# Optimization experiments

Measured on AMD Instinct MI355X. Metric: run time of the kernel, lower is better.

Reference implementation:

```python
import jax, jax.numpy as jnp
import numpy as np

K_NN = 4  # hard-coded k in get_graph_feature(x, k=4)


def _conv1(h, Wm, s, b):
    # 1x1 conv1d + folded-BN (scale/shift) + ReLU
    return jax.nn.relu(jnp.einsum('oc,bcn->bon', Wm, h) * s[:, None] + b[:, None])


def _conv2(h, Wm, s, b):
    # 1x1 conv2d + folded-BN + ReLU
    return jax.nn.relu(jnp.einsum('oc,bcnk->bonk', Wm, h) * s[:, None, None] + b[:, None, None])


def _forward(x, W_dup, s_dup, b_dup, W_c1, s_c1, b_c1,
             W2a, s2a, b2a, W2b, s2b, b2b, W2c, s2c, b2c,
             W3a, s3a, b3a, W3b, s3b, b3b, W4a, bias4a, W4b, bias4b):
    B = x.shape[0]
    h = _conv1(x, W_dup, s_dup, b_dup)           # (B,256,1024)
    h = h.reshape(B, 128, 2048)                  # duplicate points: (B,128,2048)
    h = _conv1(h, W_c1, s_c1, b_c1)              # (B,64,2048)
    g = jnp.max(h, axis=2, keepdims=True)        # max_pool1d over all 2048 -> (B,64,1)
    # knn on 64-d features: pairwise = -||xi-xj||^2, topk picks nearest (self included)
    xx = jnp.sum(h * h, axis=1, keepdims=True)   # (B,1,P)
    inner = -2.0 * jnp.einsum('bcn,bcm->bnm', h, h)
    pd = -xx - inner - jnp.swapaxes(xx, 1, 2)    # (B,P,P)
    idx = jax.lax.top_k(pd, K_NN)[1]             # (B,P,k)
    xt = jnp.swapaxes(h, 1, 2)                   # (B,P,C)
    nb = xt[jnp.arange(B)[:, None, None], idx]   # gather neighbors: (B,P,k,C)
    ctr = xt[:, :, None, :]
    feat = jnp.concatenate([nb - ctr, jnp.broadcast_to(ctr, nb.shape)], axis=-1)  # (B,P,k,2C)
    feat = jnp.transpose(feat, (0, 3, 1, 2))     # (B,128,P,k)
    feat = _conv2(feat, W2a, s2a, b2a)
    feat = _conv2(feat, W2b, s2b, b2b)
    feat = _conv2(feat, W2c, s2c, b2c)           # (B,64,P,k)
    local = jnp.max(feat, axis=3)                # max over k -> (B,64,P)
    g = _conv1(g, W3a, s3a, b3a)
    g = _conv1(g, W3b, s3b, b3b)                 # (B,128,1)
    final = jnp.concatenate([local, jnp.broadcast_to(g, (B, 128, local.shape[2]))], axis=1)  # (B,192,P)
    h4 = jax.nn.relu(jnp.einsum('oc,bcn->bon', W4a, final) + bias4a[:, None])  # (B,256,P)
    out = jnp.einsum('oc,bcn->bon', W4b, h4) + bias4b[:, None]                 # (B,3,P)
    return out


def setup_inputs() -> dict:
    key = jax.random.key(0)
    ks = list(jax.random.split(key, 30))
    W = lambda k, o, c: jax.random.normal(k, (o, c), jnp.float32) * 0.05
    sc = lambda k, c: 1.0 + 0.1 * jax.random.normal(k, (c,), jnp.float32)
    bs = lambda k, c: 0.1 * jax.random.normal(k, (c,), jnp.float32)
    return {
        'search_keypoint': jax.random.normal(ks[0], (8, 128, 1024), jnp.float32),
        'W_dup': W(ks[1], 256, 128), 's_dup': sc(ks[2], 256), 'b_dup': bs(ks[3], 256),
        'W_c1': W(ks[4], 64, 128), 's_c1': sc(ks[5], 64), 'b_c1': bs(ks[6], 64),
        'W2a': W(ks[7], 64, 128), 's2a': sc(ks[8], 64), 'b2a': bs(ks[9], 64),
        'W2b': W(ks[10], 64, 64), 's2b': sc(ks[11], 64), 'b2b': bs(ks[12], 64),
        'W2c': W(ks[13], 64, 64), 's2c': sc(ks[14], 64), 'b2c': bs(ks[15], 64),
        'W3a': W(ks[16], 128, 64), 's3a': sc(ks[17], 128), 'b3a': bs(ks[18], 128),
        'W3b': W(ks[19], 128, 128), 's3b': sc(ks[20], 128), 'b3b': bs(ks[21], 128),
        'W4a': W(ks[22], 256, 192), 'bias4a': bs(ks[23], 256),
        'W4b': W(ks[24], 3, 256), 'bias4b': bs(ks[25], 3),
    }


def reference(search_keypoint, W_dup, s_dup, b_dup, W_c1, s_c1, b_c1,
              W2a, s2a, b2a, W2b, s2b, b2b, W2c, s2c, b2c,
              W3a, s3a, b3a, W3b, s3b, b3b, W4a, bias4a, W4b, bias4b):
    return _forward(search_keypoint, W_dup, s_dup, b_dup, W_c1, s_c1, b_c1,
                    W2a, s2a, b2a, W2b, s2b, b2b, W2c, s2c, b2c,
                    W3a, s3a, b3a, W3b, s3b, b3b, W4a, bias4a, W4b, bias4b)
```

## Files before the change

kernel.cpp:

```cpp
#include <hip/hip_runtime.h>
#include <float.h>

typedef __attribute__((ext_vector_type(8))) short short8;
typedef __attribute__((ext_vector_type(4))) float f32x4;
typedef unsigned short u16;
typedef unsigned long long u64;

static constexpr size_t OFF_W     = 0;
static constexpr size_t OFF_YZ    = 131072;
static constexpr size_t OFF_Zf    = 1179648;
static constexpr size_t OFF_FEATR = 2228224;
static constexpr size_t OFF_FIN   = 6422528;
static constexpr size_t OFF_XX    = 9568256;
static constexpr size_t OFF_G     = 9584640;
static constexpr size_t OFF_G4    = 9617408;
static constexpr size_t WS_FLOATS = 9652736;

static constexpr size_t WO_DUP = 0;
static constexpr size_t WO_C1  = 32768;
static constexpr size_t WO_2A  = 40960;
static constexpr size_t WO_2B  = 49152;
static constexpr size_t WO_2C  = 53248;
static constexpr size_t WO_4A  = 57344;

__device__ __forceinline__ void gl_lds16(const void* g, void* l) {
    __builtin_amdgcn_global_load_lds(
        (const __attribute__((address_space(1))) void*)g,
        (__attribute__((address_space(3))) void*)l, 16, 0, 0);
}

__device__ __forceinline__ u16 f2bf(float x) {
    union { float f; unsigned int u; } v; v.f = x;
    unsigned int r = v.u + 0x7fffu + ((v.u >> 16) & 1u);
    return (u16)(r >> 16);
}
__device__ __forceinline__ float bf2f(u16 h) {
    union { unsigned int u; float f; } v; v.u = ((unsigned int)h) << 16;
    return v.f;
}
__device__ __forceinline__ void split2(float x, u16& h, u16& l) {
    h = f2bf(x);
    l = f2bf(x - bf2f(h));
}

__device__ __forceinline__ unsigned int fmap(float f) {
    unsigned int u = __float_as_uint(f);
    return u ^ ((unsigned int)((int)u >> 31) | 0x80000000u);
}
__device__ __forceinline__ u64 mkkey(float f, int m) {
    return ((u64)fmap(f) << 32) | (unsigned int)(2047 - m);
}
static __device__ __forceinline__ void ins4k(u64 k, u64 bk[4])
{
#pragma unroll
    for (int s = 0; s < 4; ++s) {
        bool better = k > bk[s];
        u64 t = bk[s];
        bk[s] = better ? k : bk[s];
        k = better ? t : k;
    }
}

__global__ __launch_bounds__(256) void prep(
    const float* __restrict__ W_dup, const float* __restrict__ W_c1,
    const float* __restrict__ W2a, const float* __restrict__ W2b,
    const float* __restrict__ W2c, const float* __restrict__ W4a,
    const float* __restrict__ x,
    u16* __restrict__ whi, u16* __restrict__ wlo,
    u16* __restrict__ xthi, u16* __restrict__ xtlo)
{
    __shared__ float tile[64][65];
    if (blockIdx.x < 416) {
        int t = blockIdx.x * 256 + threadIdx.x;
        float v;
        if      (t < 40960) v = (t < 32768) ? W_dup[t] : W_c1[t - 32768];
        else if (t < 53248) v = (t < 49152) ? W2a[t - 40960] : W2b[t - 49152];
        else                v = (t < 57344) ? W2c[t - 53248] : W4a[t - 57344];
        u16 h, l; split2(v, h, l);
        whi[t] = h; wlo[t] = l;
    } else {
        const int bb = blockIdx.x - 416;
        const int n0 = (bb & 15) * 64;
        const int c0 = ((bb >> 4) & 1) * 64;
        const int b  = bb >> 5;
        const int t  = threadIdx.x;
        const float* xb = x + ((size_t)b * 128 + c0) * 1024;
#pragma unroll
        for (int i = 0; i < 16; ++i) {
            int c = i * 4 + (t >> 6), n = t & 63;
            tile[c][n] = xb[(size_t)c * 1024 + n0 + n];
        }
        __syncthreads();
#pragma unroll
        for (int i = 0; i < 16; ++i) {
            int n = i * 4 + (t >> 6), c = t & 63;
            u16 h, l; split2(tile[c][n], h, l);
            const size_t o = ((size_t)b * 1024 + n0 + n) * 128 + c0 + c;
            xthi[o] = h; xtlo[o] = l;
        }
    }
}

__global__ __launch_bounds__(512) void backbone(
    const u16* __restrict__ xthi, const u16* __restrict__ xtlo,
    const u16* __restrict__ whi, const u16* __restrict__ wlo,
    const float* __restrict__ s_dup, const float* __restrict__ b_dup,
    const float* __restrict__ s_c1, const float* __restrict__ b_c1,
    u16* __restrict__ h2thi, u16* __restrict__ h2tlo,
    float* __restrict__ xxb, float* __restrict__ gp,
    float* __restrict__ y, float* __restrict__ z)
{
    const int t = threadIdx.x;
    const int wu = t >> 6;
    const int lane = t & 63;
    const int j = lane & 15, q = lane >> 4;
    const int nb = blockIdx.x;
    const int b  = blockIdx.y;
    const int n0 = nb * 16;

    __shared__ __align__(16) u16 h1h[32 * 136], h1l[32 * 136];
    __shared__ __align__(16) u16 h2h[32 * 72],  h2l[32 * 72];
    __shared__ float xxp[2][4][16];
    __shared__ float gpart[2][64];

    {
        const size_t arow = ((size_t)b * 1024 + n0 + j) * 128;
        short8 ahv[4], alv[4];
#pragma unroll
        for (int ks = 0; ks < 4; ++ks) {
            ahv[ks] = *(const short8*)(xthi + arow + q * 8 + ks * 32);
            alv[ks] = *(const short8*)(xtlo + arow + q * 8 + ks * 32);
        }
        const u16* wdh = whi + WO_DUP;
        const u16* wdl = wlo + WO_DUP;
#pragma unroll
        for (int ci = 0; ci < 2; ++ci) {
            const int ctile = wu * 2 + ci;
            const int o = ctile * 16 + j;
            f32x4 acc = (f32x4){0.f, 0.f, 0.f, 0.f};
#pragma unroll
            for (int ks = 0; ks < 4; ++ks) {
                short8 bh = *(const short8*)(wdh + (size_t)o * 128 + q * 8 + ks * 32);
                short8 bl = *(const short8*)(wdl + (size_t)o * 128 + q * 8 + ks * 32);
                acc = __builtin_amdgcn_mfma_f32_16x16x32_bf16(ahv[ks], bh, acc, 0, 0, 0);
                acc = __builtin_amdgcn_mfma_f32_16x16x32_bf16(ahv[ks], bl, acc, 0, 0, 0);
                acc = __builtin_amdgcn_mfma_f32_16x16x32_bf16(alv[ks], bh, acc, 0, 0, 0);
            }
            const float sc = s_dup[o], bi = b_dup[o];
            const int lrbase = (j & 1) * 16;
            const int col = ctile * 8 + (j >> 1);
#pragma unroll
            for (int r = 0; r < 4; ++r) {
                float v = fmaxf(acc[r] * sc + bi, 0.f);
                u16 h, l; split2(v, h, l);
                const int lr = lrbase + q * 4 + r;
                h1h[lr * 136 + col] = h;
                h1l[lr * 136 + col] = l;
            }
        }
    }
    __syncthreads();

    {
        const int g = wu >> 2, cq = wu & 3;
        short8 ahv[4], alv[4];
#pragma unroll
        for (int ks = 0; ks < 4; ++ks) {
            ahv[ks] = *(const short8*)&h1h[(g * 16 + j) * 136 + q * 8 + ks * 32];
            alv[ks] = *(const short8*)&h1l[(g * 16 + j) * 136 + q * 8 + ks * 32];
        }
        const u16* wch = whi + WO_C1;
        const u16* wcl = wlo + WO_C1;
        const int o = cq * 16 + j;
        f32x4 acc = (f32x4){0.f, 0.f, 0.f, 0.f};
#pragma unroll
        for (int ks = 0; ks < 4; ++ks) {
            short8 bh = *(const short8*)(wch + (size_t)o * 128 + q * 8 + ks * 32);
            short8 bl = *(const short8*)(wcl + (size_t)o * 128 + q * 8 + ks * 32);
            acc = __builtin_amdgcn_mfma_f32_16x16x32_bf16(ahv[ks], bh, acc, 0, 0, 0);
            acc = __builtin_amdgcn_mfma_f32_16x16x32_bf16(ahv[ks], bl, acc, 0, 0, 0);
            acc = __builtin_amdgcn_mfma_f32_16x16x32_bf16(alv[ks], bh, acc, 0, 0, 0);
        }
        const float sc = s_c1[o], bi = b_c1[o];
        float sq[4];
        float cm = -FLT_MAX;
#pragma unroll
        for (int r = 0; r < 4; ++r) {
            float v = fmaxf(acc[r] * sc + bi, 0.f);
            sq[r] = v * v;
            cm = fmaxf(cm, v);
            u16 h, l; split2(v, h, l);
            const size_t R = (size_t)b * 2048 + g * 1024 + n0 + q * 4 + r;
            h2thi[R * 64 + o] = h;
            h2tlo[R * 64 + o] = l;
            const int lr = g * 16 + q * 4 + r;
            h2h[lr * 72 + o] = h;
            h2l[lr * 72 + o] = l;
        }
#pragma unroll
        for (int r = 0; r < 4; ++r) {
#pragma unroll
            for (int mask = 1; mask < 16; mask <<= 1)
                sq[r] += __shfl_xor(sq[r], mask, 64);
        }
        if (j == 0) {
#pragma unroll
            for (int r = 0; r < 4; ++r) xxp[g][cq][q * 4 + r] = sq[r];
        }
        cm = fmaxf(cm, __shfl_xor(cm, 16, 64));
        cm = fmaxf(cm, __shfl_xor(cm, 32, 64));
        if (q == 0) gpart[g][cq * 16 + j] = cm;
    }
    __syncthreads();

    if (t < 32) {
        const int g = t >> 4, i = t & 15;
        xxb[(size_t)b * 2048 + g * 1024 + n0 + i] =
            (xxp[g][0][i] + xxp[g][1][i]) + (xxp[g][2][i] + xxp[g][3][i]);
    }
    if (t >= 64 && t < 128) {
        const int c = t - 64;
        gp[((size_t)b * 64 + nb) * 64 + c] = fmaxf(gpart[0][c], gpart[1][c]);
    }

    {
        const int g = wu >> 2, half = (wu >> 1) & 1, cg = wu & 1;
        short8 ahv[2], alv[2];
#pragma unroll
        for (int ks = 0; ks < 2; ++ks) {
            ahv[ks] = *(const short8*)&h2h[(g * 16 + j) * 72 + q * 8 + ks * 32];
            alv[ks] = *(const short8*)&h2l[(g * 16 + j) * 72 + q * 8 + ks * 32];
        }
        const u16* w2h = whi + WO_2A;
        const u16* w2l = wlo + WO_2A;
        float* dst = half ? z : y;
#pragma unroll
        for (int ci = 0; ci < 2; ++ci) {
            const int o = (cg * 2 + ci) * 16 + j;
            f32x4 acc = (f32x4){0.f, 0.f, 0.f, 0.f};
#pragma unroll
            for (int ks = 0; ks < 2; ++ks) {
                short8 bh = *(const short8*)(w2h + (size_t)o * 128 + half * 64 + q * 8 + ks * 32);
                short8 bl = *(const short8*)(w2l + (size_t)o * 128 + half * 64 + q * 8 + ks * 32);
                acc = __builtin_amdgcn_mfma_f32_16x16x32_bf16(ahv[ks], bh, acc, 0, 0, 0);
                acc = __builtin_amdgcn_mfma_f32_16x16x32_bf16(ahv[ks], bl, acc, 0, 0, 0);
                acc = __builtin_amdgcn_mfma_f32_16x16x32_bf16(alv[ks], bh, acc, 0, 0, 0);
            }
#pragma unroll
            for (int r = 0; r < 4; ++r) {
                const size_t R = (size_t)b * 2048 + g * 1024 + n0 + q * 4 + r;
                dst[R * 64 + o] = acc[r];
            }
        }
    }
}

struct __align__(16) KBuf {
    u16 hi[2048];
    u16 lo[2048];
    float xm[32];
};

__global__ __launch_bounds__(128) void knn_topk(const u16* __restrict__ thi,
                                                const u16* __restrict__ tlo,
                                                const float* __restrict__ xx,
                                                u64* __restrict__ part)
{
    const int b    = blockIdx.z;
    const int mh   = blockIdx.y;
    const int t    = threadIdx.x;
    const int wu   = __builtin_amdgcn_readfirstlane(t >> 6);
    const int lane = t & 63;
    const int j    = lane & 15;
    const int q    = lane >> 4;
    const int nrow0 = blockIdx.x * 32 + wu * 16;

    const u16* th = thi + (size_t)b * 2048 * 64;
    const u16* tl = tlo + (size_t)b * 2048 * 64;
    const float* xb = xx + (size_t)b * 2048;

    __shared__ KBuf sb[2];

    const size_t arow = (size_t)(nrow0 + j) * 64;
    short8 ah0 = *(const short8*)(th + arow + q * 8);
    short8 ah1 = *(const short8*)(th + arow + 32 + q * 8);
    short8 al0 = *(const short8*)(tl + arow + q * 8);
    short8 al1 = *(const short8*)(tl + arow + 32 + q * 8);

    u64 bk[4][4];
#pragma unroll
    for (int r = 0; r < 4; ++r)
#pragma unroll
        for (int s = 0; s < 4; ++s) bk[r][s] = 0ull;

    const int mbeg = mh * 1024;

#define KNN_STAGE(BUF, M0)                                                        \
    {                                                                             \
        _Pragma("unroll")                                                         \
        for (int ii = 0; ii < 2; ++ii) {                                          \
            const int s = (wu * 2 + ii) * 64 + lane;                              \
            const int ml = s & 31, ch = s >> 5;                                   \
            gl_lds16(th + (size_t)((M0) + ml) * 64 + ch * 8, &sb[BUF].hi[s * 8]); \
            gl_lds16(tl + (size_t)((M0) + ml) * 64 + ch * 8, &sb[BUF].lo[s * 8]); \
        }                                                                         \
        if (wu == 0 && lane < 8) gl_lds16(xb + (M0) + lane * 4, &sb[BUF].xm[0]);  \
    }

    KNN_STAGE(0, mbeg)

    for (int tt = 0; tt < 32; ++tt) {
        __syncthreads();
        if (tt < 31) KNN_STAGE((tt + 1) & 1, mbeg + (tt + 1) * 32)
        const KBuf& bf = sb[tt & 1];
        const int m0 = mbeg + tt * 32;

        float pds[2][4];
#pragma unroll
        for (int sub = 0; sub < 2; ++sub) {
            const int ml = sub * 16 + j;
            short8 bh0 = *(const short8*)&bf.hi[(q * 32 + ml) * 8];
            short8 bh1 = *(const short8*)&bf.hi[((4 + q) * 32 + ml) * 8];
            short8 bl0 = *(const short8*)&bf.lo[(q * 32 + ml) * 8];
            short8 bl1 = *(const short8*)&bf.lo[((4 + q) * 32 + ml) * 8];
            const float xmv = bf.xm[ml];
            f32x4 accA = (f32x4){0.f, 0.f, 0.f, 0.f};
            f32x4 accB = (f32x4){0.f, 0.f, 0.f, 0.f};
            accA = __builtin_amdgcn_mfma_f32_16x16x32_bf16(ah0, bh0, accA, 0, 0, 0);
            accB = __builtin_amdgcn_mfma_f32_16x16x32_bf16(ah1, bh1, accB, 0, 0, 0);
            accA = __builtin_amdgcn_mfma_f32_16x16x32_bf16(ah0, bl0, accA, 0, 0, 0);
            accB = __builtin_amdgcn_mfma_f32_16x16x32_bf16(ah1, bl1, accB, 0, 0, 0);
            accA = __builtin_amdgcn_mfma_f32_16x16x32_bf16(al0, bh0, accA, 0, 0, 0);
            accB = __builtin_amdgcn_mfma_f32_16x16x32_bf16(al1, bh1, accB, 0, 0, 0);
            accA = __builtin_amdgcn_mfma_f32_16x16x32_bf16(al0, bl0, accA, 0, 0, 0);
            accB = __builtin_amdgcn_mfma_f32_16x16x32_bf16(al1, bl1, accB, 0, 0, 0);
#pragma unroll
            for (int r = 0; r < 4; ++r)
                pds[sub][r] = __builtin_fmaf(2.f, accA[r] + accB[r], -xmv);
        }

#pragma unroll
        for (int r = 0; r < 4; ++r) {
            float mx = fmaxf(pds[0][r], pds[1][r]);
            if (fmap(mx) >= (unsigned int)(bk[r][3] >> 32)) {
#pragma unroll
                for (int sub = 0; sub < 2; ++sub) {
                    u64 key = mkkey(pds[sub][r], m0 + sub * 16 + j);
                    if (key > bk[r][3]) ins4k(key, bk[r]);
                }
            }
        }
    }
#undef KNN_STAGE

#pragma unroll
    for (int rr = 0; rr < 4; ++rr) {
#pragma unroll
        for (int mask = 1; mask < 16; mask <<= 1) {
            u64 pk[4];
#pragma unroll
            for (int s = 0; s < 4; ++s) pk[s] = __shfl_xor(bk[rr][s], mask, 64);
#pragma unroll
            for (int s = 0; s < 4; ++s) ins4k(pk[s], bk[rr]);
        }
    }
    if (j == 0) {
#pragma unroll
        for (int r = 0; r < 4; ++r) {
            const int nrow = nrow0 + q * 4 + r;
            u64* pp = part + (((size_t)b * 2 + mh) * 2048 + nrow) * 4;
            pp[0] = bk[r][0]; pp[1] = bk[r][1]; pp[2] = bk[r][2]; pp[3] = bk[r][3];
        }
    }
}

__global__ __launch_bounds__(128) void gconv_kernel(
    const float* __restrict__ gp,
    const float* __restrict__ W3a, const float* __restrict__ s3a, const float* __restrict__ b3a,
    const float* __restrict__ W3b, const float* __restrict__ s3b, const float* __restrict__ b3b,
    const float* __restrict__ W4a, float* __restrict__ g4)
{
    const int b = blockIdx.x;
    const int t = threadIdx.x;
    __shared__ float gl[64], ga[128], gb[128];
    if (t < 64) {
        float m = -FLT_MAX;
        for (int s = 0; s < 64; ++s)
            m = fmaxf(m, gp[((size_t)b * 64 + s) * 64 + t]);
        gl[t] = m;
    }
    __syncthreads();
    float a = 0.f;
#pragma unroll
    for (int c = 0; c < 64; ++c) a += W3a[t * 64 + c] * gl[c];
    ga[t] = fmaxf(a * s3a[t] + b3a[t], 0.f);
    __syncthreads();
    float o = 0.f;
#pragma unroll
    for (int c = 0; c < 128; ++c) o += W3b[t * 128 + c] * ga[c];
    gb[t] = fmaxf(o * s3b[t] + b3b[t], 0.f);
    __syncthreads();
    for (int oo = t; oo < 256; oo += 128) {
        float s = 0.f;
#pragma unroll 4
        for (int c = 0; c < 128; ++c)
            s += W4a[(size_t)oo * 192 + 64 + c] * gb[c];
        g4[(size_t)b * 256 + oo] = s;
    }
}

__global__ __launch_bounds__(256) void fused_edge(
    const u64* __restrict__ part,
    const float* __restrict__ y, const float* __restrict__ z,
    const float* __restrict__ s2a, const float* __restrict__ b2a,
    const u16* __restrict__ w2bh, const u16* __restrict__ w2bl,
    const float* __restrict__ s2b, const float* __restrict__ b2b,
    const u16* __restrict__ w2ch, const u16* __restrict__ w2cl,
    const float* __restrict__ s2c, const float* __restrict__ b2c,
    const u16* __restrict__ w4ah, const u16* __restrict__ w4al,
    const float* __restrict__ b4a, const float* __restrict__ g4,
    const float* __restrict__ W4b, const float* __restrict__ b4b,
    float* __restrict__ out)
{
    const int t = threadIdx.x;
    const int wu = t >> 6;
    const int lane = t & 63;
    const int j = lane & 15, q = lane >> 4;
    const int b = blockIdx.x >> 7;
    const int n0 = (blockIdx.x & 127) * 16;
    const int nw0 = n0 + wu * 4;

    __shared__ __align__(16) u16 plh[64 * 72];
    __shared__ __align__(16) u16 pll[64 * 72];
    __shared__ __align__(16) u16 finh[16 * 72];
    __shared__ __align__(16) u16 finl[16 * 72];
    __shared__ float pred[4][3][16];
    __shared__ int sidx[64];

    if (lane < 4) {
        const int n = nw0 + lane;
        u64 fk[4] = {0ull, 0ull, 0ull, 0ull};
#pragma unroll
        for (int qt = 0; qt < 2; ++qt) {
            const u64* pp = part + (((size_t)b * 2 + qt) * 2048 + n) * 4;
#pragma unroll
            for (int s = 0; s < 4; ++s) ins4k(pp[s], fk);
        }
        int4 ii;
        ii.x = 2047 - (int)(fk[0] & 0x7ff);
        ii.y = 2047 - (int)(fk[1] & 0x7ff);
        ii.z = 2047 - (int)(fk[2] & 0x7ff);
        ii.w = 2047 - (int)(fk[3] & 0x7ff);
        *(int4*)&sidx[wu * 16 + lane * 4] = ii;
    }

    {
        const int row = lane >> 2;
        const int c0 = (lane & 3) * 16;
        const int id = sidx[wu * 16 + row];
        const int nfull = nw0 + (row >> 2);
        const float* yb = y + (size_t)b * 2048 * 64;
        const float* yi = yb + (size_t)id * 64;
        const float* yn = yb + (size_t)nfull * 64;
        const float* zn = z + ((size_t)b * 2048 + nfull) * 64;
        u16* oh = &plh[(wu * 16 + row) * 72 + c0];
        u16* ol = &pll[(wu * 16 + row) * 72 + c0];
#pragma unroll
        for (int cc = 0; cc < 16; cc += 4) {
            const int c = c0 + cc;
            float4 a  = *(const float4*)(yi + c);
            float4 bq = *(const float4*)(yn + c);
            float4 cq = *(const float4*)(zn + c);
            float4 sv = *(const float4*)(s2a + c);
            float4 bb = *(const float4*)(b2a + c);
            float v0 = fmaxf((a.x - bq.x + cq.x) * sv.x + bb.x, 0.f);
            float v1 = fmaxf((a.y - bq.y + cq.y) * sv.y + bb.y, 0.f);
            float v2 = fmaxf((a.z - bq.z + cq.z) * sv.z + bb.z, 0.f);
            float v3 = fmaxf((a.w - bq.w + cq.w) * sv.w + bb.w, 0.f);
            union { u16 u[4]; uint2 v; } ph, pl;
            split2(v0, ph.u[0], pl.u[0]);
            split2(v1, ph.u[1], pl.u[1]);
            split2(v2, ph.u[2], pl.u[2]);
            split2(v3, ph.u[3], pl.u[3]);
            *(uint2*)(oh + cc) = ph.v;
            *(uint2*)(ol + cc) = pl.v;
        }
    }

    {
        const int abase = (wu * 16 + j) * 72 + q * 8;
        short8 ah0 = *(const short8*)&plh[abase];
        short8 ah1 = *(const short8*)&plh[abase + 32];
        short8 al0 = *(const short8*)&pll[abase];
        short8 al1 = *(const short8*)&pll[abase + 32];
#pragma unroll
        for (int ct = 0; ct < 4; ++ct) {
            const int o = ct * 16 + j;
            short8 bh0 = *(const short8*)(w2bh + (size_t)o * 64 + q * 8);
            short8 bh1 = *(const short8*)(w2bh + (size_t)o * 64 + 32 + q * 8);
            short8 bl0 = *(const short8*)(w2bl + (size_t)o * 64 + q * 8);
            short8 bl1 = *(const short8*)(w2bl + (size_t)o * 64 + 32 + q * 8);
            f32x4 acc = (f32x4){0.f, 0.f, 0.f, 0.f};
            acc = __builtin_amdgcn_mfma_f32_16x16x32_bf16(ah0, bh0, acc, 0, 0, 0);
            acc = __builtin_amdgcn_mfma_f32_16x16x32_bf16(ah0, bl0, acc, 0, 0, 0);
            acc = __builtin_amdgcn_mfma_f32_16x16x32_bf16(al0, bh0, acc, 0, 0, 0);
            acc = __builtin_amdgcn_mfma_f32_16x16x32_bf16(ah1, bh1, acc, 0, 0, 0);
            acc = __builtin_amdgcn_mfma_f32_16x16x32_bf16(ah1, bl1, acc, 0, 0, 0);
            acc = __builtin_amdgcn_mfma_f32_16x16x32_bf16(al1, bh1, acc, 0, 0, 0);
            const float sc = s2b[o], bi = b2b[o];
#pragma unroll
            for (int r = 0; r < 4; ++r) {
                float v = fmaxf(acc[r] * sc + bi, 0.f);
                u16 h, l; split2(v, h, l);
                const int row = wu * 16 + q * 4 + r;
                plh[row * 72 + o] = h;
                pll[row * 72 + o] = l;
            }
        }
    }

    {
        const int abase = (wu * 16 + j) * 72 + q * 8;
        short8 ah0 = *(const short8*)&plh[abase];
        short8 ah1 = *(const short8*)&plh[abase + 32];
        short8 al0 = *(const short8*)&pll[abase];
        short8 al1 = *(const short8*)&pll[abase + 32];
#pragma unroll
        for (int ct = 0; ct < 4; ++ct) {
            const int o = ct * 16 + j;
            short8 bh0 = *(const short8*)(w2ch + (size_t)o * 64 + q * 8);
            short8 bh1 = *(const short8*)(w2ch + (size_t)o * 64 + 32 + q * 8);
            short8 bl0 = *(const short8*)(w2cl + (size_t)o * 64 + q * 8);
            short8 bl1 = *(const short8*)(w2cl + (size_t)o * 64 + 32 + q * 8);
            f32x4 acc = (f32x4){0.f, 0.f, 0.f, 0.f};
            acc = __builtin_amdgcn_mfma_f32_16x16x32_bf16(ah0, bh0, acc, 0, 0, 0);
            acc = __builtin_amdgcn_mfma_f32_16x16x32_bf16(ah0, bl0, acc, 0, 0, 0);
            acc = __builtin_amdgcn_mfma_f32_16x16x32_bf16(al0, bh0, acc, 0, 0, 0);
            acc = __builtin_amdgcn_mfma_f32_16x16x32_bf16(ah1, bh1, acc, 0, 0, 0);
            acc = __builtin_amdgcn_mfma_f32_16x16x32_bf16(ah1, bl1, acc, 0, 0, 0);
            acc = __builtin_amdgcn_mfma_f32_16x16x32_bf16(al1, bh1, acc, 0, 0, 0);
            const float sc = s2c[o], bi = b2c[o];
            float m = -FLT_MAX;
#pragma unroll
            for (int r = 0; r < 4; ++r)
                m = fmaxf(m, fmaxf(acc[r] * sc + bi, 0.f));
            u16 h, l; split2(m, h, l);
            const int frow = wu * 4 + q;
            finh[frow * 72 + o] = h;
            finl[frow * 72 + o] = l;
        }
    }
    __syncthreads();

    {
        short8 a_hi[2], a_lo[2];
#pragma unroll
        for (int ks = 0; ks < 2; ++ks) {
            a_hi[ks] = *(const short8*)&finh[j * 72 + q * 8 + ks * 32];
            a_lo[ks] = *(const short8*)&finl[j * 72 + q * 8 + ks * 32];
        }
        float p[3][4];
#pragma unroll
        for (int oo = 0; oo < 3; ++oo)
#pragma unroll
            for (int r = 0; r < 4; ++r) p[oo][r] = 0.f;

#pragma unroll
        for (int ci = 0; ci < 4; ++ci) {
            const int o = (wu * 4 + ci) * 16 + j;
            const u16* wr_h = w4ah + (size_t)o * 192 + q * 8;
            const u16* wr_l = w4al + (size_t)o * 192 + q * 8;
            f32x4 acc = (f32x4){0.f, 0.f, 0.f, 0.f};
#pragma unroll
            for (int ks = 0; ks < 2; ++ks) {
                short8 bh = *(const short8*)(wr_h + ks * 32);
                short8 bl = *(const short8*)(wr_l + ks * 32);
                acc = __builtin_amdgcn_mfma_f32_16x16x32_bf16(a_hi[ks], bh, acc, 0, 0, 0);
                acc = __builtin_amdgcn_mfma_f32_16x16x32_bf16(a_hi[ks], bl, acc, 0, 0, 0);
                acc = __builtin_amdgcn_mfma_f32_16x16x32_bf16(a_lo[ks], bh, acc, 0, 0, 0);
            }
            const float bi = b4a[o] + g4[(size_t)b * 256 + o];
            float w0 = W4b[o], w1 = W4b[256 + o], w2 = W4b[512 + o];
#pragma unroll
            for (int r = 0; r < 4; ++r) {
                float v = fmaxf(acc[r] + bi, 0.f);
                p[0][r] += w0 * v;
                p[1][r] += w1 * v;
                p[2][r] += w2 * v;
            }
        }
#pragma unroll
        for (int oo = 0; oo < 3; ++oo)
#pragma unroll
            for (int r = 0; r < 4; ++r) {
#pragma unroll
                for (int mask = 1; mask < 16; mask <<= 1)
                    p[oo][r] += __shfl_xor(p[oo][r], mask, 64);
            }
        if (j == 0) {
#pragma unroll
            for (int oo = 0; oo < 3; ++oo)
#pragma unroll
                for (int r = 0; r < 4; ++r)
                    pred[wu][oo][q * 4 + r] = p[oo][r];
        }
    }
    __syncthreads();

    if (t < 48) {
        const int oo = t >> 4, rr = t & 15;
        float s = (pred[0][oo][rr] + pred[1][oo][rr]) +
                  (pred[2][oo][rr] + pred[3][oo][rr]) + b4b[oo];
        out[((size_t)b * 3 + oo) * 2048 + n0 + rr] = s;
    }
}

extern "C" void kernel_launch(void* const* d_in, const int* in_sizes, int n_in,
                              void* d_out, int out_size, void* d_ws, size_t ws_size,
                              hipStream_t stream)
{
    const float* x     = (const float*)d_in[0];
    const float* W_dup = (const float*)d_in[1];
    const float* s_dup = (const float*)d_in[2];
    const float* b_dup = (const float*)d_in[3];
    const float* W_c1  = (const float*)d_in[4];
    const float* s_c1  = (const float*)d_in[5];
    const float* b_c1  = (const float*)d_in[6];
    const float* W2a   = (const float*)d_in[7];
    const float* s2a   = (const float*)d_in[8];
    const float* b2a   = (const float*)d_in[9];
    const float* W2b   = (const float*)d_in[10];
    const float* s2b   = (const float*)d_in[11];
    const float* b2b   = (const float*)d_in[12];
    const float* W2c   = (const float*)d_in[13];
    const float* s2c   = (const float*)d_in[14];
    const float* b2c   = (const float*)d_in[15];
    const float* W3a   = (const float*)d_in[16];
    const float* s3a   = (const float*)d_in[17];
    const float* b3a   = (const float*)d_in[18];
    const float* W3b   = (const float*)d_in[19];
    const float* s3b   = (const float*)d_in[20];
    const float* b3b   = (const float*)d_in[21];
    const float* W4a   = (const float*)d_in[22];
    const float* b4a   = (const float*)d_in[23];
    const float* W4b   = (const float*)d_in[24];
    const float* b4b   = (const float*)d_in[25];

    if (ws_size < WS_FLOATS * sizeof(float)) return;

    float* ws = (float*)d_ws;
    u16* whi   = (u16*)(ws + OFF_W);
    u16* wlo   = whi + 131072;
    u16* xthi  = (u16*)(ws + OFF_FEATR);
    u16* xtlo  = xthi + 1048576;
    u64* part  = (u64*)(ws + OFF_FEATR);
    float* y    = ws + OFF_YZ;
    float* z    = ws + OFF_Zf;
    u16* h2thi = (u16*)(ws + OFF_FIN);
    u16* h2tlo = h2thi + 1048576;
    float* xxb  = ws + OFF_XX;
    float* gp   = ws + OFF_G;
    float* g4   = ws + OFF_G4;
    float* out  = (float*)d_out;

    prep<<<672, 256, 0, stream>>>(W_dup, W_c1, W2a, W2b, W2c, W4a, x,
                                  whi, wlo, xthi, xtlo);
    backbone<<<dim3(64, 8), 512, 0, stream>>>(
        xthi, xtlo, whi, wlo, s_dup, b_dup, s_c1, b_c1,
        h2thi, h2tlo, xxb, gp, y, z);
    gconv_kernel<<<8, 128, 0, stream>>>(gp, W3a, s3a, b3a, W3b, s3b, b3b, W4a, g4);
    knn_topk<<<dim3(64, 2, 8), 128, 0, stream>>>(h2thi, h2tlo, xxb, part);
    fused_edge<<<1024, 256, 0, stream>>>(
        part, y, z, s2a, b2a,
        whi + WO_2B, wlo + WO_2B, s2b, b2b,
        whi + WO_2C, wlo + WO_2C, s2c, b2c,
        whi + WO_4A, wlo + WO_4A, b4a, g4, W4b, b4b, out);
}
```

Before: 246.3 us.

## Fuse x transpose into backbone, merge gconv into knn, enlarge knn tiles

The input transpose and bf16 hi/lo split move from the prep kernel into the backbone kernel, which now loads x directly and stages it in LDS, removing a global round trip. The gconv kernel is folded into the knn kernel as an extra z-slice of blocks, saving one launch. The knn kernel doubles its block to 256 threads with 64-row tiles and 64-column stages, halving the loop count and changing the LDS layout. The cost is more LDS per block and possibly lower occupancy in knn.

```diff
diff --git a/kernel.cpp b/kernel.cpp
--- a/kernel.cpp
+++ b/kernel.cpp
@@ -65,44 +65,19 @@
     const float* __restrict__ W_dup, const float* __restrict__ W_c1,
     const float* __restrict__ W2a, const float* __restrict__ W2b,
     const float* __restrict__ W2c, const float* __restrict__ W4a,
+    u16* __restrict__ whi, u16* __restrict__ wlo)
+{
+    int t = blockIdx.x * 256 + threadIdx.x;
+    float v;
+    if      (t < 40960) v = (t < 32768) ? W_dup[t] : W_c1[t - 32768];
+    else if (t < 53248) v = (t < 49152) ? W2a[t - 40960] : W2b[t - 49152];
+    else                v = (t < 57344) ? W2c[t - 53248] : W4a[t - 57344];
+    u16 h, l; split2(v, h, l);
+    whi[t] = h; wlo[t] = l;
+}
+
+__global__ __launch_bounds__(512) void backbone(
     const float* __restrict__ x,
-    u16* __restrict__ whi, u16* __restrict__ wlo,
-    u16* __restrict__ xthi, u16* __restrict__ xtlo)
-{
-    __shared__ float tile[64][65];
-    if (blockIdx.x < 416) {
-        int t = blockIdx.x * 256 + threadIdx.x;
-        float v;
-        if      (t < 40960) v = (t < 32768) ? W_dup[t] : W_c1[t - 32768];
-        else if (t < 53248) v = (t < 49152) ? W2a[t - 40960] : W2b[t - 49152];
-        else                v = (t < 57344) ? W2c[t - 53248] : W4a[t - 57344];
-        u16 h, l; split2(v, h, l);
-        whi[t] = h; wlo[t] = l;
-    } else {
-        const int bb = blockIdx.x - 416;
-        const int n0 = (bb & 15) * 64;
-        const int c0 = ((bb >> 4) & 1) * 64;
-        const int b  = bb >> 5;
-        const int t  = threadIdx.x;
-        const float* xb = x + ((size_t)b * 128 + c0) * 1024;
-#pragma unroll
-        for (int i = 0; i < 16; ++i) {
-            int c = i * 4 + (t >> 6), n = t & 63;
-            tile[c][n] = xb[(size_t)c * 1024 + n0 + n];
-        }
-        __syncthreads();
-#pragma unroll
-        for (int i = 0; i < 16; ++i) {
-            int n = i * 4 + (t >> 6), c = t & 63;
-            u16 h, l; split2(tile[c][n], h, l);
-            const size_t o = ((size_t)b * 1024 + n0 + n) * 128 + c0 + c;
-            xthi[o] = h; xtlo[o] = l;
-        }
-    }
-}
-
-__global__ __launch_bounds__(512) void backbone(
-    const u16* __restrict__ xthi, const u16* __restrict__ xtlo,
     const u16* __restrict__ whi, const u16* __restrict__ wlo,
     const float* __restrict__ s_dup, const float* __restrict__ b_dup,
     const float* __restrict__ s_c1, const float* __restrict__ b_c1,
@@ -118,18 +93,29 @@
     const int b  = blockIdx.y;
     const int n0 = nb * 16;
 
+    __shared__ __align__(16) u16 xh[16 * 136], xl[16 * 136];
     __shared__ __align__(16) u16 h1h[32 * 136], h1l[32 * 136];
     __shared__ __align__(16) u16 h2h[32 * 72],  h2l[32 * 72];
     __shared__ float xxp[2][4][16];
     __shared__ float gpart[2][64];
 
     {
-        const size_t arow = ((size_t)b * 1024 + n0 + j) * 128;
+        const int c = t >> 2, i4 = (t & 3) * 4;
+        float4 xv = *(const float4*)(x + ((size_t)b * 128 + c) * 1024 + n0 + i4);
+        u16 h, l;
+        split2(xv.x, h, l); xh[(i4 + 0) * 136 + c] = h; xl[(i4 + 0) * 136 + c] = l;
+        split2(xv.y, h, l); xh[(i4 + 1) * 136 + c] = h; xl[(i4 + 1) * 136 + c] = l;
+        split2(xv.z, h, l); xh[(i4 + 2) * 136 + c] = h; xl[(i4 + 2) * 136 + c] = l;
+        split2(xv.w, h, l); xh[(i4 + 3) * 136 + c] = h; xl[(i4 + 3) * 136 + c] = l;
+    }
+    __syncthreads();
+
+    {
         short8 ahv[4], alv[4];
 #pragma unroll
         for (int ks = 0; ks < 4; ++ks) {
-            ahv[ks] = *(const short8*)(xthi + arow + q * 8 + ks * 32);
-            alv[ks] = *(const short8*)(xtlo + arow + q * 8 + ks * 32);
+            ahv[ks] = *(const short8*)&xh[j * 136 + q * 8 + ks * 32];
+            alv[ks] = *(const short8*)&xl[j * 136 + q * 8 + ks * 32];
         }
         const u16* wdh = whi + WO_DUP;
         const u16* wdl = wlo + WO_DUP;
@@ -256,16 +242,59 @@
 }
 
 struct __align__(16) KBuf {
-    u16 hi[2048];
-    u16 lo[2048];
-    float xm[32];
+    u16 hi[4096];
+    u16 lo[4096];
+    float xm[64];
 };
 
-__global__ __launch_bounds__(128) void knn_topk(const u16* __restrict__ thi,
-                                                const u16* __restrict__ tlo,
-                                                const float* __restrict__ xx,
-                                                u64* __restrict__ part)
+__global__ __launch_bounds__(256) void knn_gconv(
+    const u16* __restrict__ thi, const u16* __restrict__ tlo,
+    const float* __restrict__ xx, u64* __restrict__ part,
+    const float* __restrict__ gp,
+    const float* __restrict__ W3a, const float* __restrict__ s3a, const float* __restrict__ b3a,
+    const float* __restrict__ W3b, const float* __restrict__ s3b, const float* __restrict__ b3b,
+    const float* __restrict__ W4a, float* __restrict__ g4)
 {
+    __shared__ KBuf sb[2];
+    __shared__ float gl[64], ga[128], gbv[128];
+
+    if (blockIdx.z == 8) {
+        if (blockIdx.y != 0 || blockIdx.x >= 8) return;
+        const int b = blockIdx.x;
+        const int t = threadIdx.x;
+        if (t < 64) {
+            float m = -FLT_MAX;
+            for (int s = 0; s < 64; ++s)
+                m = fmaxf(m, gp[((size_t)b * 64 + s) * 64 + t]);
+            gl[t] = m;
+        }
+        __syncthreads();
+        if (t < 128) {
+            float a = 0.f;
+#pragma unroll
+            for (int c = 0; c < 64; ++c) a += W3a[t * 64 + c] * gl[c];
+            ga[t] = fmaxf(a * s3a[t] + b3a[t], 0.f);
+        }
+        __syncthreads();
+        if (t < 128) {
+            float o = 0.f;
+#pragma unroll
+            for (int c = 0; c < 128; ++c) o += W3b[t * 128 + c] * ga[c];
+            gbv[t] = fmaxf(o * s3b[t] + b3b[t], 0.f);
+        }
+        __syncthreads();
+        if (t < 128) {
+            for (int oo = t; oo < 256; oo += 128) {
+                float s = 0.f;
+#pragma unroll 4
+                for (int c = 0; c < 128; ++c)
+                    s += W4a[(size_t)oo * 192 + 64 + c] * gbv[c];
+                g4[(size_t)b * 256 + oo] = s;
+            }
+        }
+        return;
+    }
+
     const int b    = blockIdx.z;
     const int mh   = blockIdx.y;
     const int t    = threadIdx.x;
@@ -273,13 +302,11 @@
     const int lane = t & 63;
     const int j    = lane & 15;
     const int q    = lane >> 4;
-    const int nrow0 = blockIdx.x * 32 + wu * 16;
+    const int nrow0 = blockIdx.x * 64 + wu * 16;
 
     const u16* th = thi + (size_t)b * 2048 * 64;
     const u16* tl = tlo + (size_t)b * 2048 * 64;
     const float* xb = xx + (size_t)b * 2048;
-
-    __shared__ KBuf sb[2];
 
     const size_t arow = (size_t)(nrow0 + j) * 64;
     short8 ah0 = *(const short8*)(th + arow + q * 8);
@@ -297,32 +324,31 @@
 
 #define KNN_STAGE(BUF, M0)                                                        \
     {                                                                             \
-        _Pragma("unroll")                                                         \
-        for (int ii = 0; ii < 2; ++ii) {                                          \
-            const int s = (wu * 2 + ii) * 64 + lane;                              \
-            const int ml = s & 31, ch = s >> 5;                                   \
-            gl_lds16(th + (size_t)((M0) + ml) * 64 + ch * 8, &sb[BUF].hi[s * 8]); \
-            gl_lds16(tl + (size_t)((M0) + ml) * 64 + ch * 8, &sb[BUF].lo[s * 8]); \
-        }                                                                         \
-        if (wu == 0 && lane < 8) gl_lds16(xb + (M0) + lane * 4, &sb[BUF].xm[0]);  \
+        const u16* sh = th + (size_t)((M0) + lane) * 64;                          \
+        const u16* sl = tl + (size_t)((M0) + lane) * 64;                          \
+        gl_lds16(sh + (2 * wu) * 8,     &sb[BUF].hi[(2 * wu) * 512]);             \
+        gl_lds16(sh + (2 * wu + 1) * 8, &sb[BUF].hi[(2 * wu + 1) * 512]);         \
+        gl_lds16(sl + (2 * wu) * 8,     &sb[BUF].lo[(2 * wu) * 512]);             \
+        gl_lds16(sl + (2 * wu + 1) * 8, &sb[BUF].lo[(2 * wu + 1) * 512]);         \
+        if (wu == 0 && lane < 16) gl_lds16(xb + (M0) + lane * 4, &sb[BUF].xm[0]); \
     }
 
     KNN_STAGE(0, mbeg)
 
-    for (int tt = 0; tt < 32; ++tt) {
+    for (int tt = 0; tt < 16; ++tt) {
         __syncthreads();
-        if (tt < 31) KNN_STAGE((tt + 1) & 1, mbeg + (tt + 1) * 32)
+        if (tt < 15) KNN_STAGE((tt + 1) & 1, mbeg + (tt + 1) * 64)
         const KBuf& bf = sb[tt & 1];
-        const int m0 = mbeg + tt * 32;
-
-        float pds[2][4];
-#pragma unroll
-        for (int sub = 0; sub < 2; ++sub) {
+        const int m0 = mbeg + tt * 64;
+
+        float pds[4][4];
+#pragma unroll
+        for (int sub = 0; sub < 4; ++sub) {
             const int ml = sub * 16 + j;
-            short8 bh0 = *(const short8*)&bf.hi[(q * 32 + ml) * 8];
-            short8 bh1 = *(const short8*)&bf.hi[((4 + q) * 32 + ml) * 8];
-            short8 bl0 = *(const short8*)&bf.lo[(q * 32 + ml) * 8];
-            short8 bl1 = *(const short8*)&bf.lo[((4 + q) * 32 + ml) * 8];
+            short8 bh0 = *(const short8*)&bf.hi[(q) * 512 + ml * 8];
+            short8 bh1 = *(const short8*)&bf.hi[(4 + q) * 512 + ml * 8];
+            short8 bl0 = *(const short8*)&bf.lo[(q) * 512 + ml * 8];
+            short8 bl1 = *(const short8*)&bf.lo[(4 + q) * 512 + ml * 8];
             const float xmv = bf.xm[ml];
             f32x4 accA = (f32x4){0.f, 0.f, 0.f, 0.f};
             f32x4 accB = (f32x4){0.f, 0.f, 0.f, 0.f};
@@ -341,10 +367,10 @@
 
 #pragma unroll
         for (int r = 0; r < 4; ++r) {
-            float mx = fmaxf(pds[0][r], pds[1][r]);
+            float mx = fmaxf(fmaxf(pds[0][r], pds[1][r]), fmaxf(pds[2][r], pds[3][r]));
             if (fmap(mx) >= (unsigned int)(bk[r][3] >> 32)) {
 #pragma unroll
-                for (int sub = 0; sub < 2; ++sub) {
+                for (int sub = 0; sub < 4; ++sub) {
                     u64 key = mkkey(pds[sub][r], m0 + sub * 16 + j);
                     if (key > bk[r][3]) ins4k(key, bk[r]);
                 }
@@ -371,41 +397,6 @@
             u64* pp = part + (((size_t)b * 2 + mh) * 2048 + nrow) * 4;
             pp[0] = bk[r][0]; pp[1] = bk[r][1]; pp[2] = bk[r][2]; pp[3] = bk[r][3];
         }
-    }
-}
-
-__global__ __launch_bounds__(128) void gconv_kernel(
-    const float* __restrict__ gp,
-    const float* __restrict__ W3a, const float* __restrict__ s3a, const float* __restrict__ b3a,
-    const float* __restrict__ W3b, const float* __restrict__ s3b, const float* __restrict__ b3b,
-    const float* __restrict__ W4a, float* __restrict__ g4)
-{
-    const int b = blockIdx.x;
-    const int t = threadIdx.x;
-    __shared__ float gl[64], ga[128], gb[128];
-    if (t < 64) {
-        float m = -FLT_MAX;
-        for (int s = 0; s < 64; ++s)
-            m = fmaxf(m, gp[((size_t)b * 64 + s) * 64 + t]);
-        gl[t] = m;
-    }
-    __syncthreads();
-    float a = 0.f;
-#pragma unroll
-    for (int c = 0; c < 64; ++c) a += W3a[t * 64 + c] * gl[c];
-    ga[t] = fmaxf(a * s3a[t] + b3a[t], 0.f);
-    __syncthreads();
-    float o = 0.f;
-#pragma unroll
-    for (int c = 0; c < 128; ++c) o += W3b[t * 128 + c] * ga[c];
-    gb[t] = fmaxf(o * s3b[t] + b3b[t], 0.f);
-    __syncthreads();
-    for (int oo = t; oo < 256; oo += 128) {
-        float s = 0.f;
-#pragma unroll 4
-        for (int c = 0; c < 128; ++c)
-            s += W4a[(size_t)oo * 192 + 64 + c] * gb[c];
-        g4[(size_t)b * 256 + oo] = s;
     }
 }
 
@@ -651,8 +642,6 @@
     float* ws = (float*)d_ws;
     u16* whi   = (u16*)(ws + OFF_W);
     u16* wlo   = whi + 131072;
-    u16* xthi  = (u16*)(ws + OFF_FEATR);
-    u16* xtlo  = xthi + 1048576;
     u64* part  = (u64*)(ws + OFF_FEATR);
     float* y    = ws + OFF_YZ;
     float* z    = ws + OFF_Zf;
@@ -663,13 +652,13 @@
     float* g4   = ws + OFF_G4;
     float* out  = (float*)d_out;
 
-    prep<<<672, 256, 0, stream>>>(W_dup, W_c1, W2a, W2b, W2c, W4a, x,
-                                  whi, wlo, xthi, xtlo);
+    prep<<<416, 256, 0, stream>>>(W_dup, W_c1, W2a, W2b, W2c, W4a, whi, wlo);
     backbone<<<dim3(64, 8), 512, 0, stream>>>(
-        xthi, xtlo, whi, wlo, s_dup, b_dup, s_c1, b_c1,
+        x, whi, wlo, s_dup, b_dup, s_c1, b_c1,
         h2thi, h2tlo, xxb, gp, y, z);
-    gconv_kernel<<<8, 128, 0, stream>>>(gp, W3a, s3a, b3a, W3b, s3b, b3b, W4a, g4);
-    knn_topk<<<dim3(64, 2, 8), 128, 0, stream>>>(h2thi, h2tlo, xxb, part);
+    knn_gconv<<<dim3(32, 2, 9), 256, 0, stream>>>(
+        h2thi, h2tlo, xxb, part,
+        gp, W3a, s3a, b3a, W3b, s3b, b3b, W4a, g4);
     fused_edge<<<1024, 256, 0, stream>>>(
         part, y, z, s2a, b2a,
         whi + WO_2B, wlo + WO_2B, s2b, b2b,
```

New measurement: 219.3 us. 1.12x faster.
